# Kernel tuning notes

Measured on AMD Instinct MI355X. Metric: run time of the kernel, lower is better.

Reference implementation:

```python
import jax, jax.numpy as jnp
import numpy as np

N, D, H = 65536, 512, 256  # batch, input_dim, hidden_dim
BN_EPS = 1e-5
EPS = 1e-15


def setup_inputs() -> dict:
    key = jax.random.key(0)
    ks = jax.random.split(key, 10)
    rn = lambda k, shape, sc: jax.random.normal(k, shape, dtype=jnp.float32) * sc
    return {
        "x1": rn(ks[0], (N, D), 1.0),
        "x2": rn(ks[1], (N, D), 1.0),
        "W1": rn(ks[2], (D, H), 0.04),
        "b1": jnp.zeros((H,), jnp.float32),
        "gamma": jnp.ones((H,), jnp.float32),
        "beta_bn": jnp.zeros((H,), jnp.float32),
        "W2": rn(ks[3], (H, H // 2), 0.06),
        "b2": jnp.zeros((H // 2,), jnp.float32),
        "W3": rn(ks[4], (H // 2 * 3, 64), 0.05),
        "b3": jnp.zeros((64,), jnp.float32),
        "W4": rn(ks[5], (64, 1), 0.12),
        "b4": jnp.zeros((1,), jnp.float32),
        "alpha": jnp.array([0.65], jnp.float32),
        "beta": jnp.array([0.25], jnp.float32),
    }


def _proj(x, W1, b1, gamma, beta_bn, W2, b2):
    h = x @ W1 + b1                       # [N, 256]
    mean = jnp.mean(h, axis=0)
    var = jnp.var(h, axis=0)              # biased, matches BN training normalization
    h = gamma * (h - mean) * jax.lax.rsqrt(var + BN_EPS) + beta_bn
    h = jax.nn.relu(h)
    return jax.nn.relu(h @ W2 + b2)       # [N, 128]


def reference(x1, x2, W1, b1, gamma, beta_bn, W2, b2, W3, b3, W4, b4, alpha, beta):
    h1 = _proj(x1, W1, b1, gamma, beta_bn, W2, b2)
    h2 = _proj(x2, W1, b1, gamma, beta_bn, W2, b2)
    # diag of normalized similarity matrix == row-wise cosine similarity
    dot = jnp.sum(h1 * h2, axis=1)
    inv1 = 1.0 / jnp.maximum(jnp.sqrt(jnp.sum(h1 * h1, axis=1)), EPS)
    inv2 = 1.0 / jnp.maximum(jnp.sqrt(jnp.sum(h2 * h2, axis=1)), EPS)
    s_math = jnp.clip(dot * inv1 * inv2, 0.0, 1.0)
    combined = jnp.concatenate([h1 * h2, jnp.abs(h1 - h2), h1 + h2], axis=1)  # [N, 384]
    s_learn = (jax.nn.relu(combined @ W3 + b3) @ W4 + b4).reshape(-1)          # [N]
    final = alpha * s_math + beta * jax.nn.sigmoid(s_learn)
    return jnp.clip(final, 0.0, 1.0)
```

## Files before the change

### kernel.cpp

```cpp
#include <hip/hip_runtime.h>
#include <hip/hip_bf16.h>
#include <math.h>

#define NROWS 65536
#define DIN   512
#define H1    256
#define H2    128
#define K3DIM 384
#define O3    64

typedef short  short8  __attribute__((ext_vector_type(8)));
typedef float  f32x4   __attribute__((ext_vector_type(4)));
typedef unsigned short u16x4 __attribute__((ext_vector_type(4)));

__device__ __forceinline__ unsigned short f2bf(float f) {
    union { float f; unsigned int i; } v; v.f = f;
    unsigned int r = (v.i + 0x7fffu + ((v.i >> 16) & 1u)) >> 16;
    return (unsigned short)r;
}
__device__ __forceinline__ float bf2f(unsigned short u) {
    union { unsigned int i; float f; } v; v.i = ((unsigned int)u) << 16;
    return v.f;
}

typedef const __attribute__((address_space(1))) unsigned int* gas1_t;
typedef __attribute__((address_space(3))) unsigned int* las3_t;
__device__ __forceinline__ void gload_lds16(const void* g, void* l) {
    __builtin_amdgcn_global_load_lds((gas1_t)g, (las3_t)l, 16, 0, 0);
}

__global__ void transpose_cvt_kernel(const float* __restrict__ src,
                                     unsigned short* __restrict__ dst, int R, int C) {
    int idx = blockIdx.x * 256 + threadIdx.x;
    if (idx >= R * C) return;
    int c = idx / R, r = idx - c * R;
    dst[idx] = f2bf(src[r * C + c]);
}

#define LDA1 32

__global__ __launch_bounds__(256, 2)
void gemm1_kernel(const float* __restrict__ x1, const float* __restrict__ x2,
                  const unsigned short* __restrict__ w1t, const float* __restrict__ b1,
                  unsigned short* __restrict__ h_out, float* __restrict__ stats) {
    __shared__ __align__(1024) unsigned short Al[64 * LDA1];
    __shared__ __align__(1024) unsigned short Bl[256 * LDA1];
    const int t    = threadIdx.x;
    const int row0 = blockIdx.x * 64;
    const int inp  = row0 >> 16;
    const float* xp = inp ? x2 : x1;
    const int r0 = row0 & (NROWS - 1);

    const int wave = t >> 6, lane = t & 63;
    const int m = lane & 15, q = lane >> 4;

    const int bn_local = lane >> 2;
    const int bk_off   = (lane & 3) * 8;

    f32x4 acc[4][4] = {};

    for (int k0 = 0; k0 < DIN; k0 += 32) {
        __syncthreads();
#pragma unroll
        for (int i = 0; i < 4; ++i) {
            int chunk = wave * 4 + i;
            int n = chunk * 16 + bn_local;
            gload_lds16(w1t + (size_t)n * DIN + k0 + bk_off, &Bl[chunk * 512]);
        }
#pragma unroll
        for (int i = 0; i < 2; ++i) {
            int u = t + i * 256;
            int r = u >> 3, kq = u & 7;
            const float4 v = *reinterpret_cast<const float4*>(xp + (size_t)(r0 + r) * DIN + k0 + kq * 4);
            u16x4 b; b.x = f2bf(v.x); b.y = f2bf(v.y); b.z = f2bf(v.z); b.w = f2bf(v.w);
            *reinterpret_cast<u16x4*>(&Al[r * LDA1 + kq * 4]) = b;
        }
        __syncthreads();
        short8 af[4], bfr[4];
#pragma unroll
        for (int mi = 0; mi < 4; ++mi)
            af[mi] = *reinterpret_cast<const short8*>(&Al[(mi * 16 + m) * LDA1 + q * 8]);
#pragma unroll
        for (int ni = 0; ni < 4; ++ni)
            bfr[ni] = *reinterpret_cast<const short8*>(&Bl[(wave * 64 + ni * 16 + m) * LDA1 + q * 8]);
#pragma unroll
        for (int mi = 0; mi < 4; ++mi)
#pragma unroll
            for (int ni = 0; ni < 4; ++ni)
                acc[mi][ni] = __builtin_amdgcn_mfma_f32_16x16x32_bf16(af[mi], bfr[ni], acc[mi][ni], 0, 0, 0);
    }

#pragma unroll
    for (int ni = 0; ni < 4; ++ni) {
        const int col = wave * 64 + ni * 16 + m;
        const float bias = b1[col];
        float s = 0.f, ssq = 0.f;
#pragma unroll
        for (int mi = 0; mi < 4; ++mi) {
#pragma unroll
            for (int r = 0; r < 4; ++r) {
                int row = row0 + mi * 16 + q * 4 + r;
                float v = acc[mi][ni][r] + bias;
                h_out[(size_t)row * H1 + col] = f2bf(v);
                s += v; ssq += v * v;
            }
        }
        s   += __shfl_xor(s, 16);   s   += __shfl_xor(s, 32);
        ssq += __shfl_xor(ssq, 16); ssq += __shfl_xor(ssq, 32);
        if (q == 0) {
            atomicAdd(&stats[(inp * 2 + 0) * H1 + col], s);
            atomicAdd(&stats[(inp * 2 + 1) * H1 + col], ssq);
        }
    }
}

__global__ void bnparams_kernel(const float* __restrict__ stats, const float* __restrict__ gamma,
                                const float* __restrict__ beta_bn, float* __restrict__ ab) {
    int t = threadIdx.x;
    int inp = t >> 8, c = t & 255;
    float mean = stats[(inp * 2 + 0) * H1 + c] * (1.0f / NROWS);
    float ex2  = stats[(inp * 2 + 1) * H1 + c] * (1.0f / NROWS);
    float var  = ex2 - mean * mean;
    float a = gamma[c] * rsqrtf(var + 1e-5f);
    ab[(inp * 2 + 0) * H1 + c] = a;
    ab[(inp * 2 + 1) * H1 + c] = beta_bn[c] - a * mean;
}

#define LDA  40
#define LDB2 264

__global__ __launch_bounds__(256, 2)
void gemm2_kernel(const unsigned short* __restrict__ h, const unsigned short* __restrict__ w2t,
                  const float* __restrict__ b2, const float* __restrict__ ab,
                  unsigned short* __restrict__ z) {
    __shared__ __align__(16) unsigned short Al[128 * LDA];
    __shared__ __align__(16) unsigned short B2[128 * LDB2];
    __shared__ float sc[H1], sh[H1];
    const int t  = threadIdx.x;
    const int m0 = blockIdx.x * 128;
    const int inp = m0 >> 16;
    if (t < 256) { sc[t] = ab[(inp * 2 + 0) * H1 + t]; sh[t] = ab[(inp * 2 + 1) * H1 + t]; }
#pragma unroll
    for (int i = 0; i < 8; ++i) {
        int c = t + i * 256;
        int n = c >> 4, kc = c & 15;
        const float4* src = reinterpret_cast<const float4*>(w2t + n * H1 + kc * 16);
        float4 v0 = src[0], v1 = src[1];
        *reinterpret_cast<float4*>(&B2[n * LDB2 + kc * 16])     = v0;
        *reinterpret_cast<float4*>(&B2[n * LDB2 + kc * 16 + 8]) = v1;
    }
    const int wave = t >> 6, lane = t & 63;
    const int wm = wave >> 1, wn = wave & 1;
    const int m = lane & 15, q = lane >> 4;
    f32x4 acc[4][4] = {};
    for (int k0 = 0; k0 < H1; k0 += 32) {
        __syncthreads();
        {
            int r = t >> 1, kh = t & 1;
            const unsigned short* src = h + (size_t)(m0 + r) * H1 + k0 + kh * 16;
            unsigned short vs[16]  __attribute__((aligned(16)));
            unsigned short ob[16]  __attribute__((aligned(16)));
            *reinterpret_cast<float4*>(vs)     = *reinterpret_cast<const float4*>(src);
            *reinterpret_cast<float4*>(vs + 8) = *reinterpret_cast<const float4*>(src + 8);
#pragma unroll
            for (int j = 0; j < 16; ++j) {
                int k = k0 + kh * 16 + j;
                float v = sc[k] * bf2f(vs[j]) + sh[k];
                ob[j] = f2bf(fmaxf(v, 0.f));
            }
            *reinterpret_cast<float4*>(&Al[r * LDA + kh * 16])     = *reinterpret_cast<float4*>(ob);
            *reinterpret_cast<float4*>(&Al[r * LDA + kh * 16 + 8]) = *reinterpret_cast<float4*>(ob + 8);
        }
        __syncthreads();
        short8 af[4], bfr[4];
#pragma unroll
        for (int mi = 0; mi < 4; ++mi)
            af[mi] = *reinterpret_cast<const short8*>(&Al[(wm * 64 + mi * 16 + m) * LDA + q * 8]);
#pragma unroll
        for (int ni = 0; ni < 4; ++ni)
            bfr[ni] = *reinterpret_cast<const short8*>(&B2[(wn * 64 + ni * 16 + m) * LDB2 + k0 + q * 8]);
#pragma unroll
        for (int mi = 0; mi < 4; ++mi)
#pragma unroll
            for (int ni = 0; ni < 4; ++ni)
                acc[mi][ni] = __builtin_amdgcn_mfma_f32_16x16x32_bf16(af[mi], bfr[ni], acc[mi][ni], 0, 0, 0);
    }
#pragma unroll
    for (int mi = 0; mi < 4; ++mi)
#pragma unroll
        for (int ni = 0; ni < 4; ++ni) {
            int col = wn * 64 + ni * 16 + m;
            float bias = b2[col];
#pragma unroll
            for (int r = 0; r < 4; ++r) {
                int row = m0 + wm * 64 + mi * 16 + q * 4 + r;
                z[(size_t)row * H2 + col] = f2bf(fmaxf(acc[mi][ni][r] + bias, 0.f));
            }
        }
}

#define LDZ  136
#define LDW3 392

__global__ __launch_bounds__(512, 2)
void head_kernel(const unsigned short* __restrict__ z, const unsigned short* __restrict__ w3t,
                 const float* __restrict__ b3, const float* __restrict__ w4,
                 const float* __restrict__ b4, const float* __restrict__ alpha,
                 const float* __restrict__ beta, float* __restrict__ out) {
    __shared__ __align__(16) unsigned short Z1[128 * LDZ];
    __shared__ __align__(16) unsigned short Z2[128 * LDZ];
    __shared__ __align__(16) unsigned short W3l[64 * LDW3];
    __shared__ float b3s[64], w4s[64];
    __shared__ float smath[128], slearn[128];

    const int t  = threadIdx.x;
    const int r0 = blockIdx.x * 128;

    {
        int r = t >> 2, seg = t & 3;
        const float4* f1 = reinterpret_cast<const float4*>(z + (size_t)(r0 + r) * H2 + seg * 32);
        const float4* f2 = reinterpret_cast<const float4*>(z + (size_t)(NROWS + r0 + r) * H2 + seg * 32);
        float4* d1 = reinterpret_cast<float4*>(&Z1[r * LDZ + seg * 32]);
        float4* d2 = reinterpret_cast<float4*>(&Z2[r * LDZ + seg * 32]);
        d1[0] = f1[0]; d1[1] = f1[1]; d1[2] = f1[2]; d1[3] = f1[3];
        d2[0] = f2[0]; d2[1] = f2[1]; d2[2] = f2[2]; d2[3] = f2[3];
    }
#pragma unroll
    for (int i = 0; i < 3; ++i) {
        int c = t + i * 512;
        int n = c / 24, kc = c - n * 24;
        const float4* src = reinterpret_cast<const float4*>(w3t + n * K3DIM + kc * 16);
        float4 v0 = src[0], v1 = src[1];
        *reinterpret_cast<float4*>(&W3l[n * LDW3 + kc * 16])     = v0;
        *reinterpret_cast<float4*>(&W3l[n * LDW3 + kc * 16 + 8]) = v1;
    }
    if (t < 64) { b3s[t] = b3[t]; w4s[t] = w4[t]; }
    __syncthreads();

    {
        int r = t >> 2, part = t & 3;
        float d = 0.f, s1 = 0.f, s2 = 0.f;
#pragma unroll
        for (int j = 0; j < 32; ++j) {
            int k = part * 32 + j;
            float a = bf2f(Z1[r * LDZ + k]);
            float b = bf2f(Z2[r * LDZ + k]);
            d += a * b; s1 += a * a; s2 += b * b;
        }
        d  += __shfl_xor(d, 1);  d  += __shfl_xor(d, 2);
        s1 += __shfl_xor(s1, 1); s1 += __shfl_xor(s1, 2);
        s2 += __shfl_xor(s2, 1); s2 += __shfl_xor(s2, 2);
        if (part == 0) {
            float inv1 = 1.f / fmaxf(sqrtf(s1), 1e-15f);
            float inv2 = 1.f / fmaxf(sqrtf(s2), 1e-15f);
            float sm = d * inv1 * inv2;
            smath[r] = fminf(fmaxf(sm, 0.f), 1.f);
        }
    }

    const int wave = t >> 6, lane = t & 63;
    const int m = lane & 15, q = lane >> 4;
    const int wr = wave * 16;
    f32x4 acc[4] = {};
#pragma unroll
    for (int kb = 0; kb < 12; ++kb) {
        int seg = kb >> 2;
        int kl  = (kb & 3) * 32 + q * 8;
        short8 a1 = *reinterpret_cast<const short8*>(&Z1[(wr + m) * LDZ + kl]);
        short8 a2 = *reinterpret_cast<const short8*>(&Z2[(wr + m) * LDZ + kl]);
        short8 af;
#pragma unroll
        for (int j = 0; j < 8; ++j) {
            float v1 = bf2f((unsigned short)a1[j]);
            float v2 = bf2f((unsigned short)a2[j]);
            float v = (seg == 0) ? v1 * v2 : (seg == 1 ? fabsf(v1 - v2) : v1 + v2);
            af[j] = (short)f2bf(v);
        }
#pragma unroll
        for (int ni = 0; ni < 4; ++ni) {
            short8 bfr = *reinterpret_cast<const short8*>(&W3l[(ni * 16 + m) * LDW3 + kb * 32 + q * 8]);
            acc[ni] = __builtin_amdgcn_mfma_f32_16x16x32_bf16(af, bfr, acc[ni], 0, 0, 0);
        }
    }
    float partial[4] = {0.f, 0.f, 0.f, 0.f};
#pragma unroll
    for (int ni = 0; ni < 4; ++ni) {
        int col = ni * 16 + m;
        float bias = b3s[col], w4v = w4s[col];
#pragma unroll
        for (int rg = 0; rg < 4; ++rg) {
            float v = fmaxf(acc[ni][rg] + bias, 0.f);
            partial[rg] += v * w4v;
        }
    }
#pragma unroll
    for (int rg = 0; rg < 4; ++rg) {
        float p = partial[rg];
        p += __shfl_xor(p, 1); p += __shfl_xor(p, 2);
        p += __shfl_xor(p, 4); p += __shfl_xor(p, 8);
        if (m == 0) slearn[wr + q * 4 + rg] = p + b4[0];
    }
    __syncthreads();
    if (t < 128) {
        float sl = slearn[t];
        float sig = 1.f / (1.f + expf(-sl));
        float f = alpha[0] * smath[t] + beta[0] * sig;
        out[r0 + t] = fminf(fmaxf(f, 0.f), 1.f);
    }
}

extern "C" void kernel_launch(void* const* d_in, const int* in_sizes, int n_in,
                              void* d_out, int out_size, void* d_ws, size_t ws_size,
                              hipStream_t stream) {
    (void)in_sizes; (void)n_in; (void)out_size; (void)ws_size;
    const float* x1      = (const float*)d_in[0];
    const float* x2      = (const float*)d_in[1];
    const float* W1      = (const float*)d_in[2];
    const float* b1      = (const float*)d_in[3];
    const float* gamma   = (const float*)d_in[4];
    const float* beta_bn = (const float*)d_in[5];
    const float* W2      = (const float*)d_in[6];
    const float* b2      = (const float*)d_in[7];
    const float* W3      = (const float*)d_in[8];
    const float* b3      = (const float*)d_in[9];
    const float* W4      = (const float*)d_in[10];
    const float* b4      = (const float*)d_in[11];
    const float* alpha   = (const float*)d_in[12];
    const float* beta    = (const float*)d_in[13];
    float* out = (float*)d_out;

    char* ws = (char*)d_ws;
    unsigned short* h   = (unsigned short*)(ws);
    unsigned short* w1t = (unsigned short*)(ws + 67108864);
    unsigned short* w2t = (unsigned short*)(ws + 67371008);
    unsigned short* w3t = (unsigned short*)(ws + 67436544);
    float*          stats = (float*)(ws + 67485696);
    float*          ab    = (float*)(ws + 67489792);
    unsigned short* z   = (unsigned short*)(ws + 67493888);

    (void)hipMemsetAsync(stats, 0, 4096, stream);
    transpose_cvt_kernel<<<(DIN * H1 + 255) / 256, 256, 0, stream>>>(W1, w1t, DIN, H1);
    transpose_cvt_kernel<<<(H1 * H2 + 255) / 256, 256, 0, stream>>>(W2, w2t, H1, H2);
    transpose_cvt_kernel<<<(K3DIM * O3 + 255) / 256, 256, 0, stream>>>(W3, w3t, K3DIM, O3);
    gemm1_kernel<<<2048, 256, 0, stream>>>(x1, x2, w1t, b1, h, stats);
    bnparams_kernel<<<1, 512, 0, stream>>>(stats, gamma, beta_bn, ab);
    gemm2_kernel<<<1024, 256, 0, stream>>>(h, w2t, b2, ab, z);
    head_kernel<<<512, 512, 0, stream>>>(z, w3t, b3, W4, b4, alpha, beta, out);
}
```

Before: 388.7 us.

## Double-buffer GEMM tiles, read weights from global, merge transpose launches

gemm1 and gemm2 now use double-buffered LDS tiles with register prefetch of the next K-slice, so global loads overlap the MFMA work and one barrier per iteration is dropped. gemm2 and head_kernel no longer stage the W2/W3 weights into LDS and instead read B fragments straight from global memory (cache-resident), which cuts LDS use and the staging prologue. The three weight transpose launches are merged into one kernel. Direct global reads of the weights rely on cache hits and add register pressure.

Measured after the change: 420.5 us. +8.2%, slower.

```diff
diff --git a/kernel.cpp b/kernel.cpp
--- a/kernel.cpp
+++ b/kernel.cpp
@@ -29,12 +29,26 @@
     __builtin_amdgcn_global_load_lds((gas1_t)g, (las3_t)l, 16, 0, 0);
 }
 
-__global__ void transpose_cvt_kernel(const float* __restrict__ src,
-                                     unsigned short* __restrict__ dst, int R, int C) {
+__global__ void transpose3_kernel(const float* __restrict__ W1, const float* __restrict__ W2,
+                                  const float* __restrict__ W3,
+                                  unsigned short* __restrict__ w1t, unsigned short* __restrict__ w2t,
+                                  unsigned short* __restrict__ w3t) {
     int idx = blockIdx.x * 256 + threadIdx.x;
-    if (idx >= R * C) return;
-    int c = idx / R, r = idx - c * R;
-    dst[idx] = f2bf(src[r * C + c]);
+    const int n1 = DIN * H1;
+    const int n2 = H1 * H2;
+    const int n3 = K3DIM * O3;
+    if (idx < n1) {
+        int c = idx / DIN, r = idx - c * DIN;
+        w1t[idx] = f2bf(W1[r * H1 + c]);
+    } else if (idx < n1 + n2) {
+        int i2 = idx - n1;
+        int c = i2 / H1, r = i2 - c * H1;
+        w2t[i2] = f2bf(W2[r * H2 + c]);
+    } else if (idx < n1 + n2 + n3) {
+        int i3 = idx - n1 - n2;
+        int c = i3 / K3DIM, r = i3 - c * K3DIM;
+        w3t[i3] = f2bf(W3[r * O3 + c]);
+    }
 }
 
 #define LDA1 32
@@ -43,8 +57,8 @@
 void gemm1_kernel(const float* __restrict__ x1, const float* __restrict__ x2,
                   const unsigned short* __restrict__ w1t, const float* __restrict__ b1,
                   unsigned short* __restrict__ h_out, float* __restrict__ stats) {
-    __shared__ __align__(1024) unsigned short Al[64 * LDA1];
-    __shared__ __align__(1024) unsigned short Bl[256 * LDA1];
+    __shared__ __align__(1024) unsigned short Al[2][64 * LDA1];
+    __shared__ __align__(1024) unsigned short Bl[2][256 * LDA1];
     const int t    = threadIdx.x;
     const int row0 = blockIdx.x * 64;
     const int inp  = row0 >> 16;
@@ -56,38 +70,60 @@
 
     const int bn_local = lane >> 2;
     const int bk_off   = (lane & 3) * 8;
+    const int ar0 = t >> 3;
+    const int ak0 = (t & 7) * 4;
 
     f32x4 acc[4][4] = {};
-
-    for (int k0 = 0; k0 < DIN; k0 += 32) {
-        __syncthreads();
-#pragma unroll
-        for (int i = 0; i < 4; ++i) {
-            int chunk = wave * 4 + i;
-            int n = chunk * 16 + bn_local;
-            gload_lds16(w1t + (size_t)n * DIN + k0 + bk_off, &Bl[chunk * 512]);
-        }
-#pragma unroll
-        for (int i = 0; i < 2; ++i) {
-            int u = t + i * 256;
-            int r = u >> 3, kq = u & 7;
-            const float4 v = *reinterpret_cast<const float4*>(xp + (size_t)(r0 + r) * DIN + k0 + kq * 4);
-            u16x4 b; b.x = f2bf(v.x); b.y = f2bf(v.y); b.z = f2bf(v.z); b.w = f2bf(v.w);
-            *reinterpret_cast<u16x4*>(&Al[r * LDA1 + kq * 4]) = b;
-        }
-        __syncthreads();
+    float4 va0, va1;
+
+#pragma unroll
+    for (int i = 0; i < 4; ++i) {
+        int chunk = wave * 4 + i;
+        gload_lds16(w1t + (size_t)(chunk * 16 + bn_local) * DIN + bk_off, &Bl[0][chunk * 512]);
+    }
+    va0 = *reinterpret_cast<const float4*>(xp + (size_t)(r0 + ar0) * DIN + ak0);
+    va1 = *reinterpret_cast<const float4*>(xp + (size_t)(r0 + ar0 + 32) * DIN + ak0);
+    {
+        u16x4 c0; c0.x = f2bf(va0.x); c0.y = f2bf(va0.y); c0.z = f2bf(va0.z); c0.w = f2bf(va0.w);
+        u16x4 c1; c1.x = f2bf(va1.x); c1.y = f2bf(va1.y); c1.z = f2bf(va1.z); c1.w = f2bf(va1.w);
+        *reinterpret_cast<u16x4*>(&Al[0][ar0 * LDA1 + ak0])        = c0;
+        *reinterpret_cast<u16x4*>(&Al[0][(ar0 + 32) * LDA1 + ak0]) = c1;
+    }
+    __syncthreads();
+
+#pragma unroll
+    for (int kt = 0; kt < 16; ++kt) {
+        const int d = kt & 1;
+        if (kt < 15) {
+            const int kn = (kt + 1) * 32;
+#pragma unroll
+            for (int i = 0; i < 4; ++i) {
+                int chunk = wave * 4 + i;
+                gload_lds16(w1t + (size_t)(chunk * 16 + bn_local) * DIN + kn + bk_off,
+                            &Bl[d ^ 1][chunk * 512]);
+            }
+            va0 = *reinterpret_cast<const float4*>(xp + (size_t)(r0 + ar0) * DIN + kn + ak0);
+            va1 = *reinterpret_cast<const float4*>(xp + (size_t)(r0 + ar0 + 32) * DIN + kn + ak0);
+        }
         short8 af[4], bfr[4];
 #pragma unroll
         for (int mi = 0; mi < 4; ++mi)
-            af[mi] = *reinterpret_cast<const short8*>(&Al[(mi * 16 + m) * LDA1 + q * 8]);
+            af[mi] = *reinterpret_cast<const short8*>(&Al[d][(mi * 16 + m) * LDA1 + q * 8]);
 #pragma unroll
         for (int ni = 0; ni < 4; ++ni)
-            bfr[ni] = *reinterpret_cast<const short8*>(&Bl[(wave * 64 + ni * 16 + m) * LDA1 + q * 8]);
+            bfr[ni] = *reinterpret_cast<const short8*>(&Bl[d][(wave * 64 + ni * 16 + m) * LDA1 + q * 8]);
 #pragma unroll
         for (int mi = 0; mi < 4; ++mi)
 #pragma unroll
             for (int ni = 0; ni < 4; ++ni)
                 acc[mi][ni] = __builtin_amdgcn_mfma_f32_16x16x32_bf16(af[mi], bfr[ni], acc[mi][ni], 0, 0, 0);
+        if (kt < 15) {
+            u16x4 c0; c0.x = f2bf(va0.x); c0.y = f2bf(va0.y); c0.z = f2bf(va0.z); c0.w = f2bf(va0.w);
+            u16x4 c1; c1.x = f2bf(va1.x); c1.y = f2bf(va1.y); c1.z = f2bf(va1.z); c1.w = f2bf(va1.w);
+            *reinterpret_cast<u16x4*>(&Al[d ^ 1][ar0 * LDA1 + ak0])        = c0;
+            *reinterpret_cast<u16x4*>(&Al[d ^ 1][(ar0 + 32) * LDA1 + ak0]) = c1;
+        }
+        __syncthreads();
     }
 
 #pragma unroll
@@ -127,63 +163,89 @@
 }
 
 #define LDA  40
-#define LDB2 264
 
 __global__ __launch_bounds__(256, 2)
 void gemm2_kernel(const unsigned short* __restrict__ h, const unsigned short* __restrict__ w2t,
                   const float* __restrict__ b2, const float* __restrict__ ab,
                   unsigned short* __restrict__ z) {
-    __shared__ __align__(16) unsigned short Al[128 * LDA];
-    __shared__ __align__(16) unsigned short B2[128 * LDB2];
+    __shared__ __align__(16) unsigned short Al[2][128 * LDA];
     __shared__ float sc[H1], sh[H1];
     const int t  = threadIdx.x;
     const int m0 = blockIdx.x * 128;
     const int inp = m0 >> 16;
-    if (t < 256) { sc[t] = ab[(inp * 2 + 0) * H1 + t]; sh[t] = ab[(inp * 2 + 1) * H1 + t]; }
-#pragma unroll
-    for (int i = 0; i < 8; ++i) {
-        int c = t + i * 256;
-        int n = c >> 4, kc = c & 15;
-        const float4* src = reinterpret_cast<const float4*>(w2t + n * H1 + kc * 16);
-        float4 v0 = src[0], v1 = src[1];
-        *reinterpret_cast<float4*>(&B2[n * LDB2 + kc * 16])     = v0;
-        *reinterpret_cast<float4*>(&B2[n * LDB2 + kc * 16 + 8]) = v1;
-    }
+    sc[t] = ab[(inp * 2 + 0) * H1 + t];
+    sh[t] = ab[(inp * 2 + 1) * H1 + t];
+
     const int wave = t >> 6, lane = t & 63;
     const int wm = wave >> 1, wn = wave & 1;
     const int m = lane & 15, q = lane >> 4;
+    const int ar = t >> 1, akh = (t & 1) * 16;
+    const unsigned short* hrow = h + (size_t)(m0 + ar) * H1 + akh;
+
     f32x4 acc[4][4] = {};
-    for (int k0 = 0; k0 < H1; k0 += 32) {
-        __syncthreads();
-        {
-            int r = t >> 1, kh = t & 1;
-            const unsigned short* src = h + (size_t)(m0 + r) * H1 + k0 + kh * 16;
-            unsigned short vs[16]  __attribute__((aligned(16)));
-            unsigned short ob[16]  __attribute__((aligned(16)));
-            *reinterpret_cast<float4*>(vs)     = *reinterpret_cast<const float4*>(src);
-            *reinterpret_cast<float4*>(vs + 8) = *reinterpret_cast<const float4*>(src + 8);
+    short8 bcur[4], bnext[4];
+    float4 ha0, ha1;
+
+    ha0 = *reinterpret_cast<const float4*>(hrow);
+    ha1 = *reinterpret_cast<const float4*>(hrow + 8);
+#pragma unroll
+    for (int ni = 0; ni < 4; ++ni)
+        bcur[ni] = *reinterpret_cast<const short8*>(w2t + (size_t)(wn * 64 + ni * 16 + m) * H1 + q * 8);
+    __syncthreads();
+    {
+        unsigned short vs[16] __attribute__((aligned(16)));
+        unsigned short ob[16] __attribute__((aligned(16)));
+        *reinterpret_cast<float4*>(vs)     = ha0;
+        *reinterpret_cast<float4*>(vs + 8) = ha1;
+#pragma unroll
+        for (int j = 0; j < 16; ++j) {
+            float v = sc[akh + j] * bf2f(vs[j]) + sh[akh + j];
+            ob[j] = f2bf(fmaxf(v, 0.f));
+        }
+        *reinterpret_cast<float4*>(&Al[0][ar * LDA + akh])     = *reinterpret_cast<float4*>(ob);
+        *reinterpret_cast<float4*>(&Al[0][ar * LDA + akh + 8]) = *reinterpret_cast<float4*>(ob + 8);
+    }
+    __syncthreads();
+
+#pragma unroll
+    for (int kt = 0; kt < 8; ++kt) {
+        const int d = kt & 1;
+        if (kt < 7) {
+            const int kn = (kt + 1) * 32;
+            ha0 = *reinterpret_cast<const float4*>(hrow + kn);
+            ha1 = *reinterpret_cast<const float4*>(hrow + kn + 8);
+#pragma unroll
+            for (int ni = 0; ni < 4; ++ni)
+                bnext[ni] = *reinterpret_cast<const short8*>(
+                    w2t + (size_t)(wn * 64 + ni * 16 + m) * H1 + kn + q * 8);
+        }
+        short8 af[4];
+#pragma unroll
+        for (int mi = 0; mi < 4; ++mi)
+            af[mi] = *reinterpret_cast<const short8*>(&Al[d][(wm * 64 + mi * 16 + m) * LDA + q * 8]);
+#pragma unroll
+        for (int mi = 0; mi < 4; ++mi)
+#pragma unroll
+            for (int ni = 0; ni < 4; ++ni)
+                acc[mi][ni] = __builtin_amdgcn_mfma_f32_16x16x32_bf16(af[mi], bcur[ni], acc[mi][ni], 0, 0, 0);
+        if (kt < 7) {
+            const int kn = (kt + 1) * 32;
+            unsigned short vs[16] __attribute__((aligned(16)));
+            unsigned short ob[16] __attribute__((aligned(16)));
+            *reinterpret_cast<float4*>(vs)     = ha0;
+            *reinterpret_cast<float4*>(vs + 8) = ha1;
 #pragma unroll
             for (int j = 0; j < 16; ++j) {
-                int k = k0 + kh * 16 + j;
+                int k = kn + akh + j;
                 float v = sc[k] * bf2f(vs[j]) + sh[k];
                 ob[j] = f2bf(fmaxf(v, 0.f));
             }
-            *reinterpret_cast<float4*>(&Al[r * LDA + kh * 16])     = *reinterpret_cast<float4*>(ob);
-            *reinterpret_cast<float4*>(&Al[r * LDA + kh * 16 + 8]) = *reinterpret_cast<float4*>(ob + 8);
+            *reinterpret_cast<float4*>(&Al[d ^ 1][ar * LDA + akh])     = *reinterpret_cast<float4*>(ob);
+            *reinterpret_cast<float4*>(&Al[d ^ 1][ar * LDA + akh + 8]) = *reinterpret_cast<float4*>(ob + 8);
+#pragma unroll
+            for (int ni = 0; ni < 4; ++ni) bcur[ni] = bnext[ni];
         }
         __syncthreads();
-        short8 af[4], bfr[4];
-#pragma unroll
-        for (int mi = 0; mi < 4; ++mi)
-            af[mi] = *reinterpret_cast<const short8*>(&Al[(wm * 64 + mi * 16 + m) * LDA + q * 8]);
-#pragma unroll
-        for (int ni = 0; ni < 4; ++ni)
-            bfr[ni] = *reinterpret_cast<const short8*>(&B2[(wn * 64 + ni * 16 + m) * LDB2 + k0 + q * 8]);
-#pragma unroll
-        for (int mi = 0; mi < 4; ++mi)
-#pragma unroll
-            for (int ni = 0; ni < 4; ++ni)
-                acc[mi][ni] = __builtin_amdgcn_mfma_f32_16x16x32_bf16(af[mi], bfr[ni], acc[mi][ni], 0, 0, 0);
     }
 #pragma unroll
     for (int mi = 0; mi < 4; ++mi)
@@ -200,7 +262,6 @@
 }
 
 #define LDZ  136
-#define LDW3 392
 
 __global__ __launch_bounds__(512, 2)
 void head_kernel(const unsigned short* __restrict__ z, const unsigned short* __restrict__ w3t,
@@ -209,7 +270,6 @@
                  const float* __restrict__ beta, float* __restrict__ out) {
     __shared__ __align__(16) unsigned short Z1[128 * LDZ];
     __shared__ __align__(16) unsigned short Z2[128 * LDZ];
-    __shared__ __align__(16) unsigned short W3l[64 * LDW3];
     __shared__ float b3s[64], w4s[64];
     __shared__ float smath[128], slearn[128];
 
@@ -225,15 +285,6 @@
         d1[0] = f1[0]; d1[1] = f1[1]; d1[2] = f1[2]; d1[3] = f1[3];
         d2[0] = f2[0]; d2[1] = f2[1]; d2[2] = f2[2]; d2[3] = f2[3];
     }
-#pragma unroll
-    for (int i = 0; i < 3; ++i) {
-        int c = t + i * 512;
-        int n = c / 24, kc = c - n * 24;
-        const float4* src = reinterpret_cast<const float4*>(w3t + n * K3DIM + kc * 16);
-        float4 v0 = src[0], v1 = src[1];
-        *reinterpret_cast<float4*>(&W3l[n * LDW3 + kc * 16])     = v0;
-        *reinterpret_cast<float4*>(&W3l[n * LDW3 + kc * 16 + 8]) = v1;
-    }
     if (t < 64) { b3s[t] = b3[t]; w4s[t] = w4[t]; }
     __syncthreads();
 
@@ -278,7 +329,8 @@
         }
 #pragma unroll
         for (int ni = 0; ni < 4; ++ni) {
-            short8 bfr = *reinterpret_cast<const short8*>(&W3l[(ni * 16 + m) * LDW3 + kb * 32 + q * 8]);
+            short8 bfr = *reinterpret_cast<const short8*>(
+                w3t + (size_t)(ni * 16 + m) * K3DIM + kb * 32 + q * 8);
             acc[ni] = __builtin_amdgcn_mfma_f32_16x16x32_bf16(af, bfr, acc[ni], 0, 0, 0);
         }
     }
@@ -339,9 +391,8 @@
     unsigned short* z   = (unsigned short*)(ws + 67493888);
 
     (void)hipMemsetAsync(stats, 0, 4096, stream);
-    transpose_cvt_kernel<<<(DIN * H1 + 255) / 256, 256, 0, stream>>>(W1, w1t, DIN, H1);
-    transpose_cvt_kernel<<<(H1 * H2 + 255) / 256, 256, 0, stream>>>(W2, w2t, H1, H2);
-    transpose_cvt_kernel<<<(K3DIM * O3 + 255) / 256, 256, 0, stream>>>(W3, w3t, K3DIM, O3);
+    transpose3_kernel<<<(DIN * H1 + H1 * H2 + K3DIM * O3 + 255) / 256, 256, 0, stream>>>(
+        W1, W2, W3, w1t, w2t, w3t);
     gemm1_kernel<<<2048, 256, 0, stream>>>(x1, x2, w1t, b1, h, stats);
     bnparams_kernel<<<1, 512, 0, stream>>>(stats, gamma, beta_bn, ab);
     gemm2_kernel<<<1024, 256, 0, stream>>>(h, w2t, b2, ab, z);
```
